# Kernel tuning notes

Hardware: AMD Instinct MI355X
Metric: run time of the kernel (lower is better)

The kernel has to match this reference:

```python
import jax, jax.numpy as jnp
import numpy as np

KNOTS = 17

def _buffers():
    t = jnp.linspace(0.0, 3.0, KNOTS)                # (K,)
    dt = 3.0 / (KNOTS - 1)
    w = jnp.full((KNOTS,), 2.0 * dt)
    w = w.at[jnp.array([0, KNOTS - 1])].set(dt)      # trapezoid-like weights
    phi = jnp.exp(-t * t / 2.0)                      # standard normal CF
    return t, phi, w * phi


def setup_inputs() -> dict:
    key = jax.random.key(0)
    kz, ka = jax.random.split(key)
    n, d, num_proj = 8192, 768, 1024
    z = jax.random.normal(kz, (n, d), dtype=jnp.float32)
    a = jax.random.normal(ka, (d, num_proj), dtype=jnp.float32)
    return {"z": z, "a": a}


def reference(z, a):
    t, phi, weights = _buffers()
    # normalize projection directions (columns of a) to unit L2 norm
    a_n = a / jnp.linalg.norm(a, axis=0, keepdims=True)          # (d, P)
    proj = z @ a_n                                               # (n, P)
    x_t = proj[..., None] * t                                    # (n, P, K)
    cos_mean = jnp.cos(x_t).mean(axis=-3)                        # (P, K)
    sin_mean = jnp.sin(x_t).mean(axis=-3)                        # (P, K)
    err = (cos_mean - phi) ** 2 + sin_mean ** 2                  # (P, K)
    n = z.shape[-2]
    return (err @ weights * n).mean()                            # scalar
```

## Files before the change

kernel.cpp:

```cpp
#include <hip/hip_runtime.h>
#include <math.h>

typedef __attribute__((ext_vector_type(8))) short bf16x8;
typedef __attribute__((ext_vector_type(4))) float f32x4;

#define N_ROWS 8192
#define D_DIM  768
#define P_DIM  1024
#define KNOTS  17
#define NK     16
#define NCH    128

__device__ inline unsigned short f2bf(float f) {
    union { float f; unsigned int u; } x; x.f = f;
    unsigned int r = x.u + 0x7FFFu + ((x.u >> 16) & 1u);
    return (unsigned short)(r >> 16);
}

__device__ inline void gload_lds16(const unsigned short* g, const unsigned short* l) {
    auto gp = reinterpret_cast<const __attribute__((address_space(1))) char*>(
        reinterpret_cast<uintptr_t>(g));
    auto lp = reinterpret_cast<__attribute__((address_space(3))) char*>(
        (uintptr_t)(unsigned int)reinterpret_cast<uintptr_t>(l));
    __builtin_amdgcn_global_load_lds(gp, lp, 16, 0, 0);
}

__global__ __launch_bounds__(256) void colsq_kernel(const float* __restrict__ a,
                                                    float* __restrict__ colsq) {
    int p  = blockIdx.x * 256 + threadIdx.x;
    int d0 = blockIdx.y * 64;
    float s = 0.f;
    for (int d = 0; d < 64; ++d) {
        float v = a[(size_t)(d0 + d) * P_DIM + p];
        s = fmaf(v, v, s);
    }
    atomicAdd(&colsq[p], s);
}

__global__ __launch_bounds__(256) void zconv_kernel(const float* __restrict__ z,
                                                    unsigned short* __restrict__ zh) {
    size_t i = ((size_t)blockIdx.x * 256 + threadIdx.x) * 4;
    float4 v = *reinterpret_cast<const float4*>(z + i);
    ushort4 o;
    o.x = f2bf(v.x); o.y = f2bf(v.y); o.z = f2bf(v.z); o.w = f2bf(v.w);
    *reinterpret_cast<ushort4*>(zh + i) = o;
}

__global__ __launch_bounds__(256) void atconv_kernel(const float* __restrict__ a,
                                                     const float* __restrict__ colsq,
                                                     unsigned short* __restrict__ Bt) {
    __shared__ float tile[64][65];
    const int d0 = blockIdx.x * 64, p0 = blockIdx.y * 64;
    const int tid = threadIdx.x;
    #pragma unroll
    for (int pass = 0; pass < 16; ++pass) {
        int idx = pass * 256 + tid;
        int dr = idx >> 6, pc = idx & 63;
        tile[dr][pc] = a[(size_t)(d0 + dr) * P_DIM + p0 + pc];
    }
    __syncthreads();
    #pragma unroll
    for (int pass = 0; pass < 16; ++pass) {
        int idx = pass * 256 + tid;
        int pr = idx >> 6, dc = idx & 63;
        float inv = rsqrtf(colsq[p0 + pr]);
        Bt[(size_t)(p0 + pr) * D_DIM + d0 + dc] = f2bf(tile[dc][pr] * inv);
    }
}

__global__ __launch_bounds__(512, 4) void gemmcf_kernel(const unsigned short* __restrict__ A,
                                                        const unsigned short* __restrict__ B,
                                                        float* __restrict__ part) {
    __shared__ unsigned short As[128 * 64];
    __shared__ unsigned short Bs[128 * 64];
    const int tid  = threadIdx.x;
    const int lane = tid & 63;
    const int wave = tid >> 6;
    const int wr = wave >> 2, wc = wave & 3;

    const int bid = blockIdx.x + blockIdx.y * 8;
    const int swz = (bid & 7) * 64 + (bid >> 3);
    const int bx = swz & 7, by = swz >> 3;
    const int row0 = by * 128;
    const int col0 = bx * 128;

    const int srow  = wave * 16 + (lane >> 3);
    const int skoff = (lane & 7) * 8;
    const unsigned short* Ag = A + (size_t)(row0 + srow) * D_DIM + skoff;
    const unsigned short* Bg = B + (size_t)(col0 + srow) * D_DIM + skoff;
    const unsigned short* Asw = As + (wave * 16) * 64;
    const unsigned short* Bsw = Bs + (wave * 16) * 64;

    f32x4 acc[4][2] = {};

    for (int k0 = 0; k0 < D_DIM; k0 += 64) {
        #pragma unroll
        for (int i = 0; i < 2; ++i) {
            gload_lds16(Ag + k0 + i * (8 * D_DIM), Asw + i * (8 * 64));
            gload_lds16(Bg + k0 + i * (8 * D_DIM), Bsw + i * (8 * 64));
        }
        __syncthreads();
        #pragma unroll
        for (int kk = 0; kk < 2; ++kk) {
            bf16x8 af[4], bfr[2];
            const int kg = kk * 4 + (lane >> 4);
            #pragma unroll
            for (int mi = 0; mi < 4; ++mi)
                af[mi] = *reinterpret_cast<const bf16x8*>(
                    &As[(wr * 64 + mi * 16 + (lane & 15)) * 64 + kg * 8]);
            #pragma unroll
            for (int ni = 0; ni < 2; ++ni)
                bfr[ni] = *reinterpret_cast<const bf16x8*>(
                    &Bs[(wc * 32 + ni * 16 + (lane & 15)) * 64 + kg * 8]);
            #pragma unroll
            for (int mi = 0; mi < 4; ++mi)
                #pragma unroll
                for (int ni = 0; ni < 2; ++ni)
                    acc[mi][ni] = __builtin_amdgcn_mfma_f32_16x16x32_bf16(
                        af[mi], bfr[ni], acc[mi][ni], 0, 0, 0);
        }
        __syncthreads();
    }

    const float dt = 0.1875f;
    #pragma unroll
    for (int ni = 0; ni < 2; ++ni) {
        float cs[NK], ss[NK];
        #pragma unroll
        for (int k = 0; k < NK; ++k) { cs[k] = 0.f; ss[k] = 0.f; }
        #pragma unroll
        for (int mi = 0; mi < 4; ++mi)
            #pragma unroll
            for (int j = 0; j < 4; ++j) {
                float th = acc[mi][ni][j] * dt;
                float s1 = __sinf(th);
                float c1 = __cosf(th);
                float c2 = 2.f * c1;
                float ckm2 = 1.f, skm2 = 0.f;
                float ckm1 = c1,  skm1 = s1;
                cs[0] += c1; ss[0] += s1;
                #pragma unroll
                for (int k = 2; k <= NK; ++k) {
                    float ck = fmaf(c2, ckm1, -ckm2);
                    float sk = fmaf(c2, skm1, -skm2);
                    cs[k - 1] += ck; ss[k - 1] += sk;
                    ckm2 = ckm1; skm2 = skm1;
                    ckm1 = ck;   skm1 = sk;
                }
            }
        #pragma unroll
        for (int k = 0; k < NK; ++k) {
            cs[k] += __shfl_xor(cs[k], 16);
            cs[k] += __shfl_xor(cs[k], 32);
            ss[k] += __shfl_xor(ss[k], 16);
            ss[k] += __shfl_xor(ss[k], 32);
        }
        if (lane < 16) {
            int col = col0 + wc * 32 + ni * 16 + lane;
            size_t base = ((size_t)(by * 2 + wr) * 2 * NK) * P_DIM + col;
            #pragma unroll
            for (int k = 0; k < NK; ++k) {
                part[base + (size_t)k * P_DIM]        = cs[k];
                part[base + (size_t)(NK + k) * P_DIM] = ss[k];
            }
        }
    }
}

__global__ __launch_bounds__(256) void red1_kernel(const float* __restrict__ part,
                                                   float* __restrict__ sums) {
    int g = blockIdx.x * 256 + threadIdx.x;
    float s = 0.f;
    for (int c = 0; c < NCH; ++c)
        s += part[(size_t)c * 2 * NK * P_DIM + g];
    sums[g] = s;
}

__global__ __launch_bounds__(1024) void red2_kernel(const float* __restrict__ sums,
                                                    float* __restrict__ out) {
    const int p = threadIdx.x;
    const float dt = 0.1875f;
    const float inv_n = 1.0f / (float)N_ROWS;
    float contrib = 0.f;
    #pragma unroll
    for (int k = 1; k <= NK; ++k) {
        float cm   = sums[(k - 1) * P_DIM + p] * inv_n;
        float sm   = sums[(NK + k - 1) * P_DIM + p] * inv_n;
        float tk   = dt * (float)k;
        float phik = expf(-0.5f * tk * tk);
        float wk   = (k == KNOTS - 1) ? dt : 2.f * dt;
        float d    = cm - phik;
        contrib += wk * phik * (d * d + sm * sm);
    }
    __shared__ float red[1024];
    red[p] = contrib;
    __syncthreads();
    for (int sft = 512; sft > 0; sft >>= 1) {
        if (p < sft) red[p] += red[p + sft];
        __syncthreads();
    }
    if (p == 0) out[0] = red[0] * (float)N_ROWS / (float)P_DIM;
}

extern "C" void kernel_launch(void* const* d_in, const int* in_sizes, int n_in,
                              void* d_out, int out_size, void* d_ws, size_t ws_size,
                              hipStream_t stream) {
    const float* z = (const float*)d_in[0];
    const float* a = (const float*)d_in[1];
    float* out = (float*)d_out;

    char* ws = (char*)d_ws;
    float*          colsq = (float*)ws;
    unsigned short* zh    = (unsigned short*)(ws + 4096);
    unsigned short* Bt    = (unsigned short*)(ws + 4096 + 12582912);
    float*          part  = (float*)(ws + 4096 + 12582912 + 1572864);
    float*          sums  = (float*)(ws + 4096 + 12582912 + 1572864 + 16777216);

    hipMemsetAsync(colsq, 0, P_DIM * sizeof(float), stream);
    colsq_kernel<<<dim3(P_DIM / 256, D_DIM / 64), 256, 0, stream>>>(a, colsq);
    zconv_kernel<<<dim3(N_ROWS * D_DIM / (256 * 4)), 256, 0, stream>>>(z, zh);
    atconv_kernel<<<dim3(D_DIM / 64, P_DIM / 64), 256, 0, stream>>>(a, colsq, Bt);
    gemmcf_kernel<<<dim3(P_DIM / 128, N_ROWS / 128), 512, 0, stream>>>(zh, Bt, part);
    red1_kernel<<<dim3(2 * NK * P_DIM / 256), 256, 0, stream>>>(part, sums);
    red2_kernel<<<1, 1024, 0, stream>>>(sums, out);
}
```

Baseline: 129.0 us.

## Double-buffer GEMM LDS tiles with XOR swizzle and drop colsq memset/atomics

The GEMM main loop now double-buffers the A and B LDS tiles. It prefetches the next k-step with global_load_lds while computing the current one, using vmcnt waits and raw s_barrier in place of full __syncthreads. LDS column chunks are XOR-swizzled per row to cut bank conflicts on the MFMA fragment reads. The column-norm atomics and memset are replaced by per-block partial sums that atconv reduces into shared memory. The cost is double the LDS per block, which may lower occupancy under launch_bounds(512,4).

```diff
diff --git a/kernel.cpp b/kernel.cpp
--- a/kernel.cpp
+++ b/kernel.cpp
@@ -10,6 +10,7 @@
 #define KNOTS  17
 #define NK     16
 #define NCH    128
+#define KSTEPS 12
 
 __device__ inline unsigned short f2bf(float f) {
     union { float f; unsigned int u; } x; x.f = f;
@@ -26,7 +27,7 @@
 }
 
 __global__ __launch_bounds__(256) void colsq_kernel(const float* __restrict__ a,
-                                                    float* __restrict__ colsq) {
+                                                    float* __restrict__ cpart) {
     int p  = blockIdx.x * 256 + threadIdx.x;
     int d0 = blockIdx.y * 64;
     float s = 0.f;
@@ -34,7 +35,7 @@
         float v = a[(size_t)(d0 + d) * P_DIM + p];
         s = fmaf(v, v, s);
     }
-    atomicAdd(&colsq[p], s);
+    cpart[(size_t)blockIdx.y * P_DIM + p] = s;
 }
 
 __global__ __launch_bounds__(256) void zconv_kernel(const float* __restrict__ z,
@@ -47,11 +48,19 @@
 }
 
 __global__ __launch_bounds__(256) void atconv_kernel(const float* __restrict__ a,
-                                                     const float* __restrict__ colsq,
+                                                     const float* __restrict__ cpart,
                                                      unsigned short* __restrict__ Bt) {
     __shared__ float tile[64][65];
+    __shared__ float linv[64];
     const int d0 = blockIdx.x * 64, p0 = blockIdx.y * 64;
     const int tid = threadIdx.x;
+    if (tid < 64) {
+        float s = 0.f;
+        #pragma unroll
+        for (int j = 0; j < D_DIM / 64; ++j)
+            s += cpart[(size_t)j * P_DIM + p0 + tid];
+        linv[tid] = rsqrtf(s);
+    }
     #pragma unroll
     for (int pass = 0; pass < 16; ++pass) {
         int idx = pass * 256 + tid;
@@ -63,16 +72,15 @@
     for (int pass = 0; pass < 16; ++pass) {
         int idx = pass * 256 + tid;
         int pr = idx >> 6, dc = idx & 63;
-        float inv = rsqrtf(colsq[p0 + pr]);
-        Bt[(size_t)(p0 + pr) * D_DIM + d0 + dc] = f2bf(tile[dc][pr] * inv);
+        Bt[(size_t)(p0 + pr) * D_DIM + d0 + dc] = f2bf(tile[dc][pr] * linv[pr]);
     }
 }
 
 __global__ __launch_bounds__(512, 4) void gemmcf_kernel(const unsigned short* __restrict__ A,
                                                         const unsigned short* __restrict__ B,
                                                         float* __restrict__ part) {
-    __shared__ unsigned short As[128 * 64];
-    __shared__ unsigned short Bs[128 * 64];
+    __shared__ unsigned short AsB[2][128 * 64];
+    __shared__ unsigned short BsB[2][128 * 64];
     const int tid  = threadIdx.x;
     const int lane = tid & 63;
     const int wave = tid >> 6;
@@ -84,34 +92,45 @@
     const int row0 = by * 128;
     const int col0 = bx * 128;
 
-    const int srow  = wave * 16 + (lane >> 3);
-    const int skoff = (lane & 7) * 8;
-    const unsigned short* Ag = A + (size_t)(row0 + srow) * D_DIM + skoff;
-    const unsigned short* Bg = B + (size_t)(col0 + srow) * D_DIM + skoff;
-    const unsigned short* Asw = As + (wave * 16) * 64;
-    const unsigned short* Bsw = Bs + (wave * 16) * 64;
+    const int srow = wave * 16 + (lane >> 3);
+    const int sc   = (lane & 7) ^ ((lane >> 3) & 7);
+    const unsigned short* Ag = A + (size_t)(row0 + srow) * D_DIM + sc * 8;
+    const unsigned short* Bg = B + (size_t)(col0 + srow) * D_DIM + sc * 8;
+    const int ldsw = wave * 16 * 64;
+
+#define STAGE(kt, db)  do { const int k0_ = (kt) * 64;                       \
+        gload_lds16(Ag + k0_,             &AsB[db][ldsw]);                   \
+        gload_lds16(Ag + k0_ + 8 * D_DIM, &AsB[db][ldsw + 8 * 64]);          \
+        gload_lds16(Bg + k0_,             &BsB[db][ldsw]);                   \
+        gload_lds16(Bg + k0_ + 8 * D_DIM, &BsB[db][ldsw + 8 * 64]); } while (0)
 
     f32x4 acc[4][2] = {};
 
-    for (int k0 = 0; k0 < D_DIM; k0 += 64) {
-        #pragma unroll
-        for (int i = 0; i < 2; ++i) {
-            gload_lds16(Ag + k0 + i * (8 * D_DIM), Asw + i * (8 * 64));
-            gload_lds16(Bg + k0 + i * (8 * D_DIM), Bsw + i * (8 * 64));
-        }
-        __syncthreads();
+    STAGE(0, 0);
+    #pragma unroll
+    for (int t = 0; t < KSTEPS; ++t) {
+        const int cur = t & 1;
+        if (t + 1 < KSTEPS) {
+            STAGE(t + 1, cur ^ 1);
+            asm volatile("s_waitcnt vmcnt(4)" ::: "memory");
+        } else {
+            asm volatile("s_waitcnt vmcnt(0)" ::: "memory");
+        }
+        __builtin_amdgcn_sched_barrier(0);
+        __builtin_amdgcn_s_barrier();
         #pragma unroll
         for (int kk = 0; kk < 2; ++kk) {
             bf16x8 af[4], bfr[2];
             const int kg = kk * 4 + (lane >> 4);
+            const int kph = (kg ^ (lane & 7)) * 8;
             #pragma unroll
             for (int mi = 0; mi < 4; ++mi)
                 af[mi] = *reinterpret_cast<const bf16x8*>(
-                    &As[(wr * 64 + mi * 16 + (lane & 15)) * 64 + kg * 8]);
+                    &AsB[cur][(wr * 64 + mi * 16 + (lane & 15)) * 64 + kph]);
             #pragma unroll
             for (int ni = 0; ni < 2; ++ni)
                 bfr[ni] = *reinterpret_cast<const bf16x8*>(
-                    &Bs[(wc * 32 + ni * 16 + (lane & 15)) * 64 + kg * 8]);
+                    &BsB[cur][(wc * 32 + ni * 16 + (lane & 15)) * 64 + kph]);
             #pragma unroll
             for (int mi = 0; mi < 4; ++mi)
                 #pragma unroll
@@ -119,8 +138,9 @@
                     acc[mi][ni] = __builtin_amdgcn_mfma_f32_16x16x32_bf16(
                         af[mi], bfr[ni], acc[mi][ni], 0, 0, 0);
         }
-        __syncthreads();
-    }
+        __builtin_amdgcn_s_barrier();
+    }
+#undef STAGE
 
     const float dt = 0.1875f;
     #pragma unroll
@@ -210,16 +230,15 @@
     float* out = (float*)d_out;
 
     char* ws = (char*)d_ws;
-    float*          colsq = (float*)ws;
-    unsigned short* zh    = (unsigned short*)(ws + 4096);
-    unsigned short* Bt    = (unsigned short*)(ws + 4096 + 12582912);
-    float*          part  = (float*)(ws + 4096 + 12582912 + 1572864);
-    float*          sums  = (float*)(ws + 4096 + 12582912 + 1572864 + 16777216);
-
-    hipMemsetAsync(colsq, 0, P_DIM * sizeof(float), stream);
-    colsq_kernel<<<dim3(P_DIM / 256, D_DIM / 64), 256, 0, stream>>>(a, colsq);
+    float*          cpart = (float*)ws;
+    unsigned short* zh    = (unsigned short*)(ws + 65536);
+    unsigned short* Bt    = (unsigned short*)(ws + 65536 + 12582912);
+    float*          part  = (float*)(ws + 65536 + 12582912 + 1572864);
+    float*          sums  = (float*)(ws + 65536 + 12582912 + 1572864 + 16777216);
+
+    colsq_kernel<<<dim3(P_DIM / 256, D_DIM / 64), 256, 0, stream>>>(a, cpart);
     zconv_kernel<<<dim3(N_ROWS * D_DIM / (256 * 4)), 256, 0, stream>>>(z, zh);
-    atconv_kernel<<<dim3(D_DIM / 64, P_DIM / 64), 256, 0, stream>>>(a, colsq, Bt);
+    atconv_kernel<<<dim3(D_DIM / 64, P_DIM / 64), 256, 0, stream>>>(a, cpart, Bt);
     gemmcf_kernel<<<dim3(P_DIM / 128, N_ROWS / 128), 512, 0, stream>>>(zh, Bt, part);
     red1_kernel<<<dim3(2 * NK * P_DIM / 256), 256, 0, stream>>>(part, sums);
     red2_kernel<<<1, 1024, 0, stream>>>(sums, out);
```

After: 120.8 us. -6.3%, faster.
